# Performance work log

Hardware: AMD Instinct MI355X
Metric: run time of the kernel (lower is better)

The kernel has to match this reference:

```python
import jax, jax.numpy as jnp
import numpy as np

NUM_EXPERTS = 8
HIDDEN = 2048
INTER = 4096
TOKENS = 8192
TOP_K = 2


def relu2(x):
    # Nemotron-H 'relu2': squared ReLU
    r = jax.nn.relu(x)
    return r * r


def setup_inputs() -> dict:
    key = jax.random.key(0)
    k1, k2, k3, k4, k5 = jax.random.split(key, 5)
    hidden_states = jax.random.normal(k1, (TOKENS, HIDDEN), dtype=jnp.float32)
    top_k_index = jax.random.randint(k2, (TOKENS, TOP_K), 0, NUM_EXPERTS, dtype=jnp.int64)
    top_k_weights = jax.random.uniform(k3, (TOKENS, TOP_K), dtype=jnp.float32)
    up_proj = jax.random.normal(k4, (NUM_EXPERTS, INTER, HIDDEN), dtype=jnp.float32) * 0.02
    down_proj = jax.random.normal(k5, (NUM_EXPERTS, HIDDEN, INTER), dtype=jnp.float32) * 0.02
    return {
        "hidden_states": hidden_states,
        "top_k_index": top_k_index,
        "top_k_weights": top_k_weights,
        "up_proj": up_proj,
        "down_proj": down_proj,
    }


def reference(hidden_states, top_k_index, top_k_weights, up_proj, down_proj):
    num_experts = up_proj.shape[0]
    # combine weight per (token, expert): sum over top-k slots routed to that expert
    # (equivalent to the one-hot mask + per-slot top_k_weights in the torch loop)
    onehot = (top_k_index[:, :, None] == jnp.arange(num_experts)[None, None, :])  # [T, K, E]
    combine = jnp.sum(onehot * top_k_weights[:, :, None], axis=1)  # [T, E]
    out = jnp.zeros_like(hidden_states)
    # fixed small loop over experts (structural, not a data dim)
    for e in range(num_experts):
        h = relu2(hidden_states @ up_proj[e].T)  # [T, I]
        y = h @ down_proj[e].T  # [T, H]
        out = out + combine[:, e:e + 1] * y
    return out
```

## Files before the change

kernel.cpp:

```cpp
#include <hip/hip_runtime.h>

#define T_TOKENS 8192
#define H_DIM    2048
#define I_DIM    4096
#define NE       8
#define NPAIR    16384
#define PADBM    256
#define PADP     (NPAIR + NE * PADBM)
#define RT_MAX   (PADP / PADBM)

#define BM2 256
#define BN2 256
#define BK2 64
#define NTHR 512
#define NKT_UP (H_DIM / BK2)
#define NKT_DN (I_DIM / BK2)
#define NTN_UP (I_DIM / BN2)
#define NTN_DN (H_DIM / BN2)
#define TILE_B 32768
#define TILE_S 16384

#define G_UP   (RT_MAX * NTN_UP)
#define G_CVTD (NE * NTN_DN * NKT_DN)

#define AB_BYTES  ((size_t)RT_MAX * NKT_UP * TILE_B)
#define W_BYTES   ((size_t)NE * I_DIM * H_DIM * 2)
#define HB_BYTES  ((size_t)RT_MAX * NKT_DN * TILE_B)
#define TOK_BYTES ((size_t)PADP * 4)

typedef __attribute__((ext_vector_type(8))) short bf16x8;
typedef __attribute__((ext_vector_type(4))) float f32x4;

__device__ __forceinline__ unsigned short f2bf(float f) {
  union { float f; unsigned u; } a; a.f = f;
  unsigned r = a.u + 0x7fffu + ((a.u >> 16) & 1u);
  return (unsigned short)(r >> 16);
}

__device__ __forceinline__ float b2f(unsigned short b) {
  union { unsigned u; float f; } a; a.u = ((unsigned)b) << 16;
  return a.f;
}

__device__ __forceinline__ bf16x8 pack8(float4 a, float4 b) {
  bf16x8 o;
  o[0] = (short)f2bf(a.x); o[1] = (short)f2bf(a.y);
  o[2] = (short)f2bf(a.z); o[3] = (short)f2bf(a.w);
  o[4] = (short)f2bf(b.x); o[5] = (short)f2bf(b.y);
  o[6] = (short)f2bf(b.z); o[7] = (short)f2bf(b.w);
  return o;
}

__device__ __forceinline__ void gload16(const void* g, void* l) {
  __builtin_amdgcn_global_load_lds(
      (const __attribute__((address_space(1))) unsigned int*)g,
      (__attribute__((address_space(3))) unsigned int*)l,
      16, 0, 0);
}

__device__ __forceinline__ int swz(int a) { return a ^ ((a >> 2) & 0x60); }

__global__ __launch_bounds__(512) void route_all(const int* __restrict__ idx,
                                                 int* __restrict__ meta,
                                                 int* __restrict__ tok) {
  __shared__ int cnt[NE], base[NE + 1], cur[NE];
  int t = threadIdx.x;
  if (t < NE) { cnt[t] = 0; cur[t] = 0; }
  for (int i = t; i < PADP; i += 512) tok[i] = -1;
  __syncthreads();
  for (int i = t; i < NPAIR; i += 512) atomicAdd(&cnt[idx[i]], 1);
  __syncthreads();
  if (t == 0) {
    int off = 0;
    for (int e = 0; e < NE; ++e) {
      base[e] = off;
      off += ((cnt[e] + PADBM - 1) / PADBM) * PADBM;
    }
    base[NE] = off;
    for (int e = 0; e <= NE; ++e) meta[16 + e] = base[e];
  }
  __syncthreads();
  for (int i = t; i < NPAIR; i += 512) {
    int e = idx[i];
    int pos = base[e] + atomicAdd(&cur[e], 1);
    tok[pos] = i;
  }
}

__device__ __forceinline__ void cvt_tile_body(
    const float* __restrict__ W, unsigned short* __restrict__ out,
    int tile, int NKT, int K, char* lt) {
  int kt = tile % NKT, panel = tile / NKT;
  int t = threadIdx.x, r = t >> 1, half = t & 1;
  const float* src = W + ((size_t)panel * 256 + r) * K + kt * 64 + half * 32;
  float4 v[8];
  #pragma unroll
  for (int i = 0; i < 8; ++i) v[i] = ((const float4*)src)[i];
  #pragma unroll
  for (int i2 = 0; i2 < 4; ++i2) {
    int c = half * 4 + i2;
    *(bf16x8*)(lt + swz(c * 4096 + r * 16)) = pack8(v[2 * i2], v[2 * i2 + 1]);
  }
  __syncthreads();
  char* dst = (char*)(out + (size_t)tile * TILE_S);
  int tb = t * 16;
  #pragma unroll
  for (int i = 0; i < 4; ++i) {
    int o = i * 8192 + tb;
    *(bf16x8*)(dst + o) = *(const bf16x8*)(lt + swz(o));
  }
}

__global__ __launch_bounds__(512) void cvt_tile_w(
    const float* __restrict__ W, unsigned short* __restrict__ out,
    int NKT, int K) {
  __shared__ float4 ltq[TILE_B / 16];
  cvt_tile_body(W, out, blockIdx.x, NKT, K, (char*)ltq);
}

__global__ __launch_bounds__(512) void gather_tile_x(
    const float* __restrict__ x, const int* __restrict__ tok,
    unsigned short* __restrict__ out) {
  __shared__ float4 ltq[TILE_B / 16];
  char* lt = (char*)ltq;
  int kt = blockIdx.x & (NKT_UP - 1), rt = blockIdx.x >> 5;
  int t = threadIdx.x, r = t >> 1, half = t & 1;
  int v = tok[rt * 256 + r];
  bf16x8 pk[4];
  if (v < 0) {
    #pragma unroll
    for (int i2 = 0; i2 < 4; ++i2) pk[i2] = (bf16x8)0;
  } else {
    const float* src = x + (size_t)(v >> 1) * H_DIM + kt * 64 + half * 32;
    float4 w[8];
    #pragma unroll
    for (int i = 0; i < 8; ++i) w[i] = ((const float4*)src)[i];
    #pragma unroll
    for (int i2 = 0; i2 < 4; ++i2) pk[i2] = pack8(w[2 * i2], w[2 * i2 + 1]);
  }
  #pragma unroll
  for (int i2 = 0; i2 < 4; ++i2) {
    int c = half * 4 + i2;
    *(bf16x8*)(lt + swz(c * 4096 + r * 16)) = pk[i2];
  }
  __syncthreads();
  char* dst = (char*)(out + (size_t)blockIdx.x * TILE_S);
  int tb = t * 16;
  #pragma unroll
  for (int i = 0; i < 4; ++i) {
    int o = i * 8192 + tb;
    *(bf16x8*)(dst + o) = *(const bf16x8*)(lt + swz(o));
  }
}


#define STAGE_FULL(KT, BS) do {                                                \
    const char* aT_ = aTile + (size_t)(KT) * TILE_B;                           \
    const char* bT_ = bTile + (size_t)(KT) * TILE_B;                           \
    _Pragma("unroll")                                                          \
    for (int l_ = 0; l_ < 4; ++l_) {                                           \
      int off_ = (l_ * 8 + wv) * 1024 + lane16;                                \
      gload16(aT_ + off_, smem + (BS) * 32768 + off_);                         \
      gload16(bT_ + off_, smem + 65536 + (BS) * 32768 + off_);                 \
    }                                                                          \
  } while (0)

#define STAGE_Q(KT, BS, Q) do {                                                \
    const char* aT_ = aTile + (size_t)(KT) * TILE_B;                           \
    const char* bT_ = bTile + (size_t)(KT) * TILE_B;                           \
    int off_ = ((Q) * 8 + wv) * 1024 + lane16;                                 \
    gload16(aT_ + off_, smem + (BS) * 32768 + off_);                           \
    gload16(bT_ + off_, smem + 65536 + (BS) * 32768 + off_);                   \
  } while (0)

#define PHASE(KS, FH, DO_STAGE, DO_VM) do {                                    \
    bf16x8 af[4];                                                              \
    const char* aB_ = smem + bufc * 32768 + ((KS) * 4 + hi) * 4096;            \
    _Pragma("unroll")                                                          \
    for (int f = 0; f < 4; ++f)                                                \
      af[f] = *(const bf16x8*)(aB_ + arow_b + ((FH) * 4 + f) * 256);           \
    if ((FH) == 0) {                                                           \
      const char* bB_ = smem + 65536 + bufc * 32768 + ((KS) * 4 + hi) * 4096;  \
      _Pragma("unroll")                                                        \
      for (int f = 0; f < 4; ++f)                                              \
        bfr[f] = *(const bf16x8*)(bB_ + brow_b + f * 256);                     \
    }                                                                          \
    DO_STAGE;                                                                  \
    DO_VM;                                                                     \
    __builtin_amdgcn_s_barrier();                                              \
    asm volatile("s_waitcnt lgkmcnt(0)" ::: "memory");                         \
    __builtin_amdgcn_s_setprio(1);                                             \
    _Pragma("unroll")                                                          \
    for (int fm = 0; fm < 4; ++fm)                                             \
      _Pragma("unroll")                                                        \
      for (int fn = 0; fn < 4; ++fn)                                           \
        acc[(FH) * 4 + fm][fn] = __builtin_amdgcn_mfma_f32_16x16x32_bf16(      \
            af[fm], bfr[fn], acc[(FH) * 4 + fm][fn], 0, 0, 0);                 \
    __builtin_amdgcn_s_setprio(0);                                             \
    __builtin_amdgcn_s_barrier();                                              \
  } while (0)

#define GEMM_PROLOGUE()                                                        \
  STAGE_FULL(0, 0);                                                            \
  asm volatile("s_waitcnt vmcnt(4)" ::: "memory");                             \
  __builtin_amdgcn_s_barrier();

#define GEMM_MAIN(NKT)                                                         \
  int bufc = 0;                                                                \
  for (int kt = 0; kt < (NKT); ++kt) {                                         \
    int ktn = (kt + 1 < (NKT)) ? kt + 1 : (NKT) - 1;  \
    int bn_ = bufc ^ 1;                                                        \
    PHASE(0, 0, STAGE_Q(ktn, bn_, 0), (void)0);                                \
    PHASE(0, 1, STAGE_Q(ktn, bn_, 1),                                          \
          asm volatile("s_waitcnt vmcnt(4)" ::: "memory"));                    \
    PHASE(1, 0, STAGE_Q(ktn, bn_, 2), (void)0);                                \
    PHASE(1, 1, STAGE_Q(ktn, bn_, 3),                                          \
          asm volatile("s_waitcnt vmcnt(4)" ::: "memory"));                    \
    bufc ^= 1;                                                                 \
  }

__device__ __forceinline__ void rt_nt_decode(int bid, int NTN, int& rt, int& nt) {
  int xcd = bid & 7, g = bid >> 3;
  int gh = NTN >> 1;
  int gn = g % gh, gr = g / gh;
  rt = gr * 4 + (xcd >> 1);
  nt = gn * 2 + (xcd & 1);
}

__global__ __launch_bounds__(NTHR, 2) void gemm_up8f(
    const unsigned short* __restrict__ Ab, const unsigned short* __restrict__ WtU,
    unsigned short* __restrict__ Hb, const int* __restrict__ meta,
    const float* __restrict__ dnW, unsigned short* __restrict__ WtD,
    int nGemm) {
  extern __shared__ char smem[];
  if ((int)blockIdx.x >= nGemm) {
    cvt_tile_body(dnW, WtD, (int)blockIdx.x - nGemm, NKT_DN, I_DIM, smem);
    return;
  }
  const int* pstart = meta + 16;
  int rt, nt;
  rt_nt_decode(blockIdx.x, NTN_UP, rt, nt);
  int row0 = rt * BM2;
  if (row0 >= pstart[NE]) return;
  int e = 0;
  #pragma unroll
  for (int q = 1; q < NE; ++q) if (row0 >= pstart[q]) e = q;

  int tid = threadIdx.x;
  int wv = tid >> 6, lane = tid & 63;
  int lane16 = lane * 16;

  const char* aTile = (const char*)Ab + (size_t)rt * NKT_UP * TILE_B;
  const char* bTile = (const char*)WtU + (size_t)(e * NTN_UP + nt) * NKT_UP * TILE_B;

  int wm = wv >> 2, wn = wv & 3;
  int hi = lane >> 4;
  int arow_b = (wm * 128 + (lane & 15)) * 16;
  int brow_b = (wn * 64 + (lane & 15)) * 16;

  f32x4 acc[8][4] = {};
  bf16x8 bfr[4];

  GEMM_PROLOGUE();
  GEMM_MAIN(NKT_UP);

  unsigned short* baseT = Hb + ((size_t)rt * NKT_DN + nt * 4 + wn) * TILE_S
                             + ((lane & 15) >> 3) * 2048 + (lane & 7);
  #pragma unroll
  for (int fm = 0; fm < 8; ++fm) {
    #pragma unroll
    for (int j = 0; j < 4; ++j) {
      int r = wm * 128 + hi * 4 + fm * 16 + j;
      unsigned short* rb = baseT + r * 8;
      #pragma unroll
      for (int fn = 0; fn < 4; ++fn) {
        float v = acc[fm][fn][j];
        v = v > 0.f ? v * v : 0.f;
        rb[fn * 4096] = f2bf(v);
      }
    }
  }
}

__global__ __launch_bounds__(NTHR, 2) void gemm_down8(
    const unsigned short* __restrict__ Hb, const unsigned short* __restrict__ Wt,
    unsigned short* __restrict__ Yb, const int* __restrict__ meta,
    const int* __restrict__ tok) {
  extern __shared__ char smem[];
  const int* pstart = meta + 16;
  int rt, nt;
  rt_nt_decode(blockIdx.x, NTN_DN, rt, nt);
  int row0 = rt * BM2;
  if (row0 >= pstart[NE]) return;
  int e = 0;
  #pragma unroll
  for (int q = 1; q < NE; ++q) if (row0 >= pstart[q]) e = q;

  int tid = threadIdx.x;
  int wv = tid >> 6, lane = tid & 63;
  int lane16 = lane * 16;

  const char* aTile = (const char*)Hb + (size_t)rt * NKT_DN * TILE_B;
  const char* bTile = (const char*)Wt + (size_t)(e * NTN_DN + nt) * NKT_DN * TILE_B;

  int wm = wv >> 2, wn = wv & 3;
  int hi = lane >> 4;
  int arow_b = (wm * 128 + (lane & 15)) * 16;
  int brow_b = (wn * 64 + (lane & 15)) * 16;

  f32x4 acc[8][4] = {};
  bf16x8 bfr[4];

  GEMM_PROLOGUE();
  GEMM_MAIN(NKT_DN);

  int crow0 = row0 + wm * 128 + hi * 4;
  int ccol0 = nt * BN2 + wn * 64 + (lane & 15);
  #pragma unroll
  for (int fm = 0; fm < 8; ++fm) {
    #pragma unroll
    for (int j = 0; j < 4; ++j) {
      int p = crow0 + fm * 16 + j;
      int i = tok[p];
      if (i < 0) continue;
      unsigned short* dst = Yb + (size_t)i * H_DIM + ccol0;
      #pragma unroll
      for (int fn = 0; fn < 4; ++fn)
        dst[fn * 16] = f2bf(acc[fm][fn][j]);
    }
  }
}

__global__ __launch_bounds__(256) void combine(
    const unsigned short* __restrict__ Yb, const float* __restrict__ tkw,
    float* __restrict__ out) {
  int h0 = threadIdx.x * 8;
  #pragma unroll
  for (int tt = 0; tt < 4; ++tt) {
    int t = blockIdx.x * 4 + tt;
    float w0 = tkw[2 * t], w1 = tkw[2 * t + 1];
    bf16x8 ya = *(const bf16x8*)(Yb + (size_t)(2 * t) * H_DIM + h0);
    bf16x8 yb = *(const bf16x8*)(Yb + (size_t)(2 * t + 1) * H_DIM + h0);
    float* dst = out + (size_t)t * H_DIM + h0;
    float4 o0, o1;
    o0.x = w0 * b2f((unsigned short)ya[0]) + w1 * b2f((unsigned short)yb[0]);
    o0.y = w0 * b2f((unsigned short)ya[1]) + w1 * b2f((unsigned short)yb[1]);
    o0.z = w0 * b2f((unsigned short)ya[2]) + w1 * b2f((unsigned short)yb[2]);
    o0.w = w0 * b2f((unsigned short)ya[3]) + w1 * b2f((unsigned short)yb[3]);
    o1.x = w0 * b2f((unsigned short)ya[4]) + w1 * b2f((unsigned short)yb[4]);
    o1.y = w0 * b2f((unsigned short)ya[5]) + w1 * b2f((unsigned short)yb[5]);
    o1.z = w0 * b2f((unsigned short)ya[6]) + w1 * b2f((unsigned short)yb[6]);
    o1.w = w0 * b2f((unsigned short)ya[7]) + w1 * b2f((unsigned short)yb[7]);
    ((float4*)dst)[0] = o0;
    ((float4*)dst)[1] = o1;
  }
}

extern "C" void kernel_launch(void* const* d_in, const int* in_sizes, int n_in,
                              void* d_out, int out_size, void* d_ws, size_t ws_size,
                              hipStream_t stream) {
  const float* x   = (const float*)d_in[0];
  const int*   tki = (const int*)d_in[1];
  const float* tkw = (const float*)d_in[2];
  const float* up  = (const float*)d_in[3];
  const float* dn  = (const float*)d_in[4];
  float* out = (float*)d_out;
  char* ws = (char*)d_ws;

  size_t need_fused = AB_BYTES + 2 * W_BYTES + HB_BYTES + TOK_BYTES + 128;
  bool fused = ws_size >= need_fused;

  unsigned short* ab  = (unsigned short*)ws;
  unsigned short* wtU = (unsigned short*)(ws + AB_BYTES);
  unsigned short* wtD = fused ? (unsigned short*)(ws + AB_BYTES + W_BYTES) : wtU;
  char* pHB = (char*)wtD + W_BYTES;
  unsigned short* hb  = (unsigned short*)pHB;
  int*            tok = (int*)(pHB + HB_BYTES);
  int*            meta= (int*)(pHB + HB_BYTES + TOK_BYTES);
  unsigned short* yb  = ab;

  hipFuncSetAttribute((const void*)gemm_up8f,
                      hipFuncAttributeMaxDynamicSharedMemorySize, 131072);
  hipFuncSetAttribute((const void*)gemm_down8,
                      hipFuncAttributeMaxDynamicSharedMemorySize, 131072);

  route_all<<<1, 512, 0, stream>>>(tki, meta, tok);

  gather_tile_x<<<RT_MAX * NKT_UP, 512, 0, stream>>>(x, tok, ab);
  cvt_tile_w<<<NE * NTN_UP * NKT_UP, 512, 0, stream>>>(up, wtU, NKT_UP, H_DIM);

  if (fused) {
    gemm_up8f<<<G_UP + G_CVTD, NTHR, 131072, stream>>>(ab, wtU, hb, meta,
                                                       dn, wtD, G_UP);
  } else {
    gemm_up8f<<<G_UP, NTHR, 131072, stream>>>(ab, wtU, hb, meta, dn, wtD, G_UP);
    cvt_tile_w<<<G_CVTD, 512, 0, stream>>>(dn, wtD, NKT_DN, I_DIM);
  }

  gemm_down8<<<RT_MAX * NTN_DN, NTHR, 131072, stream>>>(hb, wtD, yb, meta, tok);

  combine<<<T_TOKENS / 4, 256, 0, stream>>>(yb, tkw, out);
}
```

Before: 823.9 us.

## Merge up and down GEMMs into persistent kernel with dependency counters

Adds a persistent mega kernel of 256 blocks. The blocks pull tasks from an atomic queue in order: up-projection tiles, down-weight conversion tiles, then down-projection tiles. Each down tile spins on per-row-tile and per-weight-tile completion counters, so it can start as soon as its inputs are ready instead of waiting for a full kernel boundary. The intent is to remove the tail and launch gap between the up and down phases. In exchange it runs at one block per CU (launch_bounds 1) rather than two, and adds spin-wait overhead and a separate Yb buffer.

```diff
diff --git a/kernel.cpp b/kernel.cpp
--- a/kernel.cpp
+++ b/kernel.cpp
@@ -22,10 +22,12 @@
 
 #define G_UP   (RT_MAX * NTN_UP)
 #define G_CVTD (NE * NTN_DN * NKT_DN)
+#define G_DN   (RT_MAX * NTN_DN)
 
 #define AB_BYTES  ((size_t)RT_MAX * NKT_UP * TILE_B)
 #define W_BYTES   ((size_t)NE * I_DIM * H_DIM * 2)
 #define HB_BYTES  ((size_t)RT_MAX * NKT_DN * TILE_B)
+#define YB_BYTES  ((size_t)NPAIR * H_DIM * 2)
 #define TOK_BYTES ((size_t)PADP * 4)
 
 typedef __attribute__((ext_vector_type(8))) short bf16x8;
@@ -60,12 +62,29 @@
 
 __device__ __forceinline__ int swz(int a) { return a ^ ((a >> 2) & 0x60); }
 
+__device__ __forceinline__ int expert_of(int row0, const int* pstart) {
+  int e = 0;
+  #pragma unroll
+  for (int q = 1; q < NE; ++q) if (row0 >= pstart[q]) e = q;
+  return e;
+}
+
+__device__ __forceinline__ void rt_nt_decode(int bid, int NTN, int& rt, int& nt) {
+  int xcd = bid & 7, g = bid >> 3;
+  int gh = NTN >> 1;
+  int gn = g % gh, gr = g / gh;
+  rt = gr * 4 + (xcd >> 1);
+  nt = gn * 2 + (xcd & 1);
+}
+
 __global__ __launch_bounds__(512) void route_all(const int* __restrict__ idx,
                                                  int* __restrict__ meta,
-                                                 int* __restrict__ tok) {
+                                                 int* __restrict__ tok,
+                                                 int* __restrict__ ctrs) {
   __shared__ int cnt[NE], base[NE + 1], cur[NE];
   int t = threadIdx.x;
   if (t < NE) { cnt[t] = 0; cur[t] = 0; }
+  if (t < 256) ctrs[t] = 0;
   for (int i = t; i < PADP; i += 512) tok[i] = -1;
   __syncthreads();
   for (int i = t; i < NPAIR; i += 512) atomicAdd(&cnt[idx[i]], 1);
@@ -152,7 +171,6 @@
     *(bf16x8*)(dst + o) = *(const bf16x8*)(lt + swz(o));
   }
 }
-
 
 #define STAGE_FULL(KT, BS) do {                                                \
     const char* aT_ = aTile + (size_t)(KT) * TILE_B;                           \
@@ -219,51 +237,23 @@
     bufc ^= 1;                                                                 \
   }
 
-__device__ __forceinline__ void rt_nt_decode(int bid, int NTN, int& rt, int& nt) {
-  int xcd = bid & 7, g = bid >> 3;
-  int gh = NTN >> 1;
-  int gn = g % gh, gr = g / gh;
-  rt = gr * 4 + (xcd >> 1);
-  nt = gn * 2 + (xcd & 1);
-}
-
-__global__ __launch_bounds__(NTHR, 2) void gemm_up8f(
+__device__ __forceinline__ void up_tile_body(
+    int rt, int nt, int e,
     const unsigned short* __restrict__ Ab, const unsigned short* __restrict__ WtU,
-    unsigned short* __restrict__ Hb, const int* __restrict__ meta,
-    const float* __restrict__ dnW, unsigned short* __restrict__ WtD,
-    int nGemm) {
-  extern __shared__ char smem[];
-  if ((int)blockIdx.x >= nGemm) {
-    cvt_tile_body(dnW, WtD, (int)blockIdx.x - nGemm, NKT_DN, I_DIM, smem);
-    return;
-  }
-  const int* pstart = meta + 16;
-  int rt, nt;
-  rt_nt_decode(blockIdx.x, NTN_UP, rt, nt);
-  int row0 = rt * BM2;
-  if (row0 >= pstart[NE]) return;
-  int e = 0;
-  #pragma unroll
-  for (int q = 1; q < NE; ++q) if (row0 >= pstart[q]) e = q;
-
+    unsigned short* __restrict__ Hb, char* smem) {
   int tid = threadIdx.x;
   int wv = tid >> 6, lane = tid & 63;
   int lane16 = lane * 16;
-
   const char* aTile = (const char*)Ab + (size_t)rt * NKT_UP * TILE_B;
   const char* bTile = (const char*)WtU + (size_t)(e * NTN_UP + nt) * NKT_UP * TILE_B;
-
   int wm = wv >> 2, wn = wv & 3;
   int hi = lane >> 4;
   int arow_b = (wm * 128 + (lane & 15)) * 16;
   int brow_b = (wn * 64 + (lane & 15)) * 16;
-
   f32x4 acc[8][4] = {};
   bf16x8 bfr[4];
-
   GEMM_PROLOGUE();
   GEMM_MAIN(NKT_UP);
-
   unsigned short* baseT = Hb + ((size_t)rt * NKT_DN + nt * 4 + wn) * TILE_S
                              + ((lane & 15) >> 3) * 2048 + (lane & 7);
   #pragma unroll
@@ -282,38 +272,24 @@
   }
 }
 
-__global__ __launch_bounds__(NTHR, 2) void gemm_down8(
-    const unsigned short* __restrict__ Hb, const unsigned short* __restrict__ Wt,
-    unsigned short* __restrict__ Yb, const int* __restrict__ meta,
-    const int* __restrict__ tok) {
-  extern __shared__ char smem[];
-  const int* pstart = meta + 16;
-  int rt, nt;
-  rt_nt_decode(blockIdx.x, NTN_DN, rt, nt);
-  int row0 = rt * BM2;
-  if (row0 >= pstart[NE]) return;
-  int e = 0;
-  #pragma unroll
-  for (int q = 1; q < NE; ++q) if (row0 >= pstart[q]) e = q;
-
+__device__ __forceinline__ void down_tile_body(
+    int rt, int nt, int e,
+    const unsigned short* __restrict__ Hb, const unsigned short* __restrict__ WtD,
+    unsigned short* __restrict__ Yb, const int* __restrict__ tok, char* smem) {
   int tid = threadIdx.x;
   int wv = tid >> 6, lane = tid & 63;
   int lane16 = lane * 16;
-
   const char* aTile = (const char*)Hb + (size_t)rt * NKT_DN * TILE_B;
-  const char* bTile = (const char*)Wt + (size_t)(e * NTN_DN + nt) * NKT_DN * TILE_B;
-
+  const char* bTile = (const char*)WtD + (size_t)(e * NTN_DN + nt) * NKT_DN * TILE_B;
   int wm = wv >> 2, wn = wv & 3;
   int hi = lane >> 4;
   int arow_b = (wm * 128 + (lane & 15)) * 16;
   int brow_b = (wn * 64 + (lane & 15)) * 16;
-
   f32x4 acc[8][4] = {};
   bf16x8 bfr[4];
-
   GEMM_PROLOGUE();
   GEMM_MAIN(NKT_DN);
-
+  int row0 = rt * BM2;
   int crow0 = row0 + wm * 128 + hi * 4;
   int ccol0 = nt * BN2 + wn * 64 + (lane & 15);
   #pragma unroll
@@ -329,6 +305,100 @@
         dst[fn * 16] = f2bf(acc[fm][fn][j]);
     }
   }
+}
+
+__global__ __launch_bounds__(NTHR, 1) void mega_updown(
+    const unsigned short* __restrict__ Ab, const unsigned short* __restrict__ WtU,
+    unsigned short* __restrict__ Hb, const float* __restrict__ dnW,
+    unsigned short* __restrict__ WtD, unsigned short* __restrict__ Yb,
+    const int* __restrict__ tok, const int* __restrict__ meta,
+    int* __restrict__ ctrs) {
+  extern __shared__ char smem[];
+  __shared__ int sTask;
+  const int* pstart = meta + 16;
+  int* done_up = ctrs + 8;
+  int* done_cv = ctrs + 96;
+  int tid = threadIdx.x;
+  for (;;) {
+    __syncthreads();
+    if (tid == 0) sTask = atomicAdd(ctrs, 1);
+    __syncthreads();
+    int task = sTask;
+    if (task < G_UP) {
+      int rt, nt;
+      rt_nt_decode(task, NTN_UP, rt, nt);
+      if (rt * BM2 < pstart[NE]) {
+        int e = expert_of(rt * BM2, pstart);
+        up_tile_body(rt, nt, e, Ab, WtU, Hb, smem);
+        __syncthreads();
+        if (tid == 0) {
+          __threadfence();
+          __hip_atomic_fetch_add(&done_up[rt], 1, __ATOMIC_RELEASE,
+                                 __HIP_MEMORY_SCOPE_AGENT);
+        }
+      }
+    } else if (task < G_UP + G_CVTD) {
+      int j = task - G_UP;
+      cvt_tile_body(dnW, WtD, j, NKT_DN, I_DIM, smem);
+      __syncthreads();
+      if (tid == 0) {
+        __threadfence();
+        __hip_atomic_fetch_add(&done_cv[j / NKT_DN], 1, __ATOMIC_RELEASE,
+                               __HIP_MEMORY_SCOPE_AGENT);
+      }
+    } else if (task < G_UP + G_CVTD + G_DN) {
+      int d = task - G_UP - G_CVTD;
+      int rt, nt;
+      rt_nt_decode(d, NTN_DN, rt, nt);
+      if (rt * BM2 < pstart[NE]) {
+        int e = expert_of(rt * BM2, pstart);
+        if (tid == 0) {
+          while (__hip_atomic_load(&done_up[rt], __ATOMIC_ACQUIRE,
+                                   __HIP_MEMORY_SCOPE_AGENT) < NTN_UP)
+            __builtin_amdgcn_s_sleep(2);
+          while (__hip_atomic_load(&done_cv[e * NTN_DN + nt], __ATOMIC_ACQUIRE,
+                                   __HIP_MEMORY_SCOPE_AGENT) < NKT_DN)
+            __builtin_amdgcn_s_sleep(2);
+          __threadfence();
+        }
+        __syncthreads();
+        down_tile_body(rt, nt, e, Hb, WtD, Yb, tok, smem);
+      }
+    } else {
+      break;
+    }
+  }
+}
+
+__global__ __launch_bounds__(NTHR, 2) void gemm_up8f(
+    const unsigned short* __restrict__ Ab, const unsigned short* __restrict__ WtU,
+    unsigned short* __restrict__ Hb, const int* __restrict__ meta,
+    const float* __restrict__ dnW, unsigned short* __restrict__ WtD,
+    int nGemm) {
+  extern __shared__ char smem[];
+  if ((int)blockIdx.x >= nGemm) {
+    cvt_tile_body(dnW, WtD, (int)blockIdx.x - nGemm, NKT_DN, I_DIM, smem);
+    return;
+  }
+  const int* pstart = meta + 16;
+  int rt, nt;
+  rt_nt_decode(blockIdx.x, NTN_UP, rt, nt);
+  if (rt * BM2 >= pstart[NE]) return;
+  int e = expert_of(rt * BM2, pstart);
+  up_tile_body(rt, nt, e, Ab, WtU, Hb, smem);
+}
+
+__global__ __launch_bounds__(NTHR, 2) void gemm_down8(
+    const unsigned short* __restrict__ Hb, const unsigned short* __restrict__ Wt,
+    unsigned short* __restrict__ Yb, const int* __restrict__ meta,
+    const int* __restrict__ tok) {
+  extern __shared__ char smem[];
+  const int* pstart = meta + 16;
+  int rt, nt;
+  rt_nt_decode(blockIdx.x, NTN_DN, rt, nt);
+  if (rt * BM2 >= pstart[NE]) return;
+  int e = expert_of(rt * BM2, pstart);
+  down_tile_body(rt, nt, e, Hb, Wt, Yb, tok, smem);
 }
 
 __global__ __launch_bounds__(256) void combine(
@@ -367,37 +437,48 @@
   float* out = (float*)d_out;
   char* ws = (char*)d_ws;
 
-  size_t need_fused = AB_BYTES + 2 * W_BYTES + HB_BYTES + TOK_BYTES + 128;
+  size_t need_mega  = AB_BYTES + 2 * W_BYTES + HB_BYTES + YB_BYTES + TOK_BYTES + 4096;
+  size_t need_fused = AB_BYTES + 2 * W_BYTES + HB_BYTES + TOK_BYTES + 4096;
+  bool mega  = ws_size >= need_mega;
   bool fused = ws_size >= need_fused;
 
-  unsigned short* ab  = (unsigned short*)ws;
-  unsigned short* wtU = (unsigned short*)(ws + AB_BYTES);
-  unsigned short* wtD = fused ? (unsigned short*)(ws + AB_BYTES + W_BYTES) : wtU;
-  char* pHB = (char*)wtD + W_BYTES;
-  unsigned short* hb  = (unsigned short*)pHB;
-  int*            tok = (int*)(pHB + HB_BYTES);
-  int*            meta= (int*)(pHB + HB_BYTES + TOK_BYTES);
-  unsigned short* yb  = ab;
-
+  char* p = ws;
+  unsigned short* ab  = (unsigned short*)p; p += AB_BYTES;
+  unsigned short* wtU = (unsigned short*)p; p += W_BYTES;
+  unsigned short* wtD = fused ? (unsigned short*)p : wtU;
+  if (fused) p += W_BYTES;
+  unsigned short* hb  = (unsigned short*)p; p += HB_BYTES;
+  unsigned short* yb;
+  if (mega) { yb = (unsigned short*)p; p += YB_BYTES; }
+  else        yb = ab;
+  int* tok  = (int*)p; p += TOK_BYTES;
+  int* ctrs = (int*)p;
+  int* meta = ctrs + 256;
+
+  hipFuncSetAttribute((const void*)mega_updown,
+                      hipFuncAttributeMaxDynamicSharedMemorySize, 131072);
   hipFuncSetAttribute((const void*)gemm_up8f,
                       hipFuncAttributeMaxDynamicSharedMemorySize, 131072);
   hipFuncSetAttribute((const void*)gemm_down8,
                       hipFuncAttributeMaxDynamicSharedMemorySize, 131072);
 
-  route_all<<<1, 512, 0, stream>>>(tki, meta, tok);
+  route_all<<<1, 512, 0, stream>>>(tki, meta, tok, ctrs);
 
   gather_tile_x<<<RT_MAX * NKT_UP, 512, 0, stream>>>(x, tok, ab);
   cvt_tile_w<<<NE * NTN_UP * NKT_UP, 512, 0, stream>>>(up, wtU, NKT_UP, H_DIM);
 
-  if (fused) {
+  if (mega) {
+    mega_updown<<<256, NTHR, 131072, stream>>>(ab, wtU, hb, dn, wtD, yb,
+                                               tok, meta, ctrs);
+  } else if (fused) {
     gemm_up8f<<<G_UP + G_CVTD, NTHR, 131072, stream>>>(ab, wtU, hb, meta,
                                                        dn, wtD, G_UP);
+    gemm_down8<<<G_DN, NTHR, 131072, stream>>>(hb, wtD, yb, meta, tok);
   } else {
     gemm_up8f<<<G_UP, NTHR, 131072, stream>>>(ab, wtU, hb, meta, dn, wtD, G_UP);
     cvt_tile_w<<<G_CVTD, 512, 0, stream>>>(dn, wtD, NKT_DN, I_DIM);
-  }
-
-  gemm_down8<<<RT_MAX * NTN_DN, NTHR, 131072, stream>>>(hb, wtD, yb, meta, tok);
+    gemm_down8<<<G_DN, NTHR, 131072, stream>>>(hb, wtD, yb, meta, tok);
+  }
 
   combine<<<T_TOKENS / 4, 256, 0, stream>>>(yb, tkw, out);
 }
```

Measured after the change: 2.652 ms. 222% more time.
